# Kernel optimization log

Hardware: AMD Instinct MI355X
Metric: run time of the kernel (lower is better)

## Reference

```python
import jax, jax.numpy as jnp
import numpy as np
import math

B, S = 2, 2048
V, D, H, L, DFF = 1024, 512, 8, 6, 2048
DK = D // H
EPS = 1e-5


def _pos_encoding(seq_len, d_model, dtype):
    pos = jnp.arange(seq_len, dtype=jnp.float32)[:, None]
    div = jnp.exp(jnp.arange(0, d_model, 2, dtype=jnp.float32) * (-math.log(10000.0) / d_model))
    pe = jnp.zeros((seq_len, d_model), dtype=jnp.float32)
    pe = pe.at[:, 0::2].set(jnp.sin(pos * div))
    pe = pe.at[:, 1::2].set(jnp.cos(pos * div))
    return pe.astype(dtype)


def _layernorm(x, w, b):
    mu = jnp.mean(x, axis=-1, keepdims=True)
    var = jnp.mean(jnp.square(x - mu), axis=-1, keepdims=True)
    return (x - mu) * jax.lax.rsqrt(var + EPS) * w + b


def setup_inputs() -> dict:
    key = jax.random.key(0)
    ks = jax.random.split(key, 20)
    s = 0.02
    inp = {
        "input_ids": jax.random.randint(ks[0], (B, S), 1, V),
        "emb": jax.random.normal(ks[1], (V, D)) * s,
        # linear weights stored (in, out) so y = x @ W + b
        "wq": jax.random.normal(ks[2], (L, D, D)) * s,
        "bq": jnp.zeros((L, D)),
        "wk": jax.random.normal(ks[3], (L, D, D)) * s,
        "bk": jnp.zeros((L, D)),
        "wv": jax.random.normal(ks[4], (L, D, D)) * s,
        "bv": jnp.zeros((L, D)),
        "wo": jax.random.normal(ks[5], (L, D, D)) * (s / math.sqrt(2 * L)),
        "bo": jnp.zeros((L, D)),
        "ln1_w": jnp.ones((L, D)), "ln1_b": jnp.zeros((L, D)),
        "ln2_w": jnp.ones((L, D)), "ln2_b": jnp.zeros((L, D)),
        "w1": jax.random.normal(ks[6], (L, D, DFF)) * s,
        "b1": jnp.zeros((L, DFF)),
        "w2": jax.random.normal(ks[7], (L, DFF, D)) * (s / math.sqrt(2 * L)),
        "b2": jnp.zeros((L, D)),
        "out_w": jax.random.normal(ks[8], (D, V)) * s,
        "out_b": jnp.zeros((V,)),
    }
    return inp


def reference(input_ids, emb, wq, bq, wk, bk, wv, bv, wo, bo,
              ln1_w, ln1_b, ln2_w, ln2_b, w1, b1, w2, b2, out_w, out_b):
    pad_mask = (input_ids != 0)                              # [B,S] attend where True
    x = emb[input_ids]                                       # [B,S,D]
    x = x + _pos_encoding(S, D, x.dtype)[None, :, :]
    causal = jnp.tril(jnp.ones((S, S), dtype=bool))          # [S,S]
    mask = causal[None, None, :, :] & pad_mask[:, None, None, :]  # [B,1,S,S]
    scale = 1.0 / math.sqrt(DK)
    for l in range(L):
        h = _layernorm(x, ln1_w[l], ln1_b[l])
        q = (h @ wq[l] + bq[l]).reshape(B, S, H, DK)
        k = (h @ wk[l] + bk[l]).reshape(B, S, H, DK)
        v = (h @ wv[l] + bv[l]).reshape(B, S, H, DK)
        scores = jnp.einsum('bqhd,bkhd->bhqk', q, k) * scale
        scores = jnp.where(mask, scores, -jnp.inf)
        attn = jax.nn.softmax(scores, axis=-1)
        o = jnp.einsum('bhqk,bkhd->bqhd', attn, v).reshape(B, S, D)
        x = o @ wo[l] + bo[l]                                # NOTE: no residual on attention (faithful)
        h2 = _layernorm(x, ln2_w[l], ln2_b[l])
        ff = jax.nn.relu(h2 @ w1[l] + b1[l]) @ w2[l] + b2[l]
        x = x + ff
    logits = x @ out_w + out_b                               # [B,S,V]
    return logits
```

## Files before the change

kernel.cpp:

```cpp
#include <hip/hip_runtime.h>
#include <hip/hip_bf16.h>

#define B_ 2
#define S_ 2048
#define V_ 1024
#define D_ 512
#define H_ 8
#define L_ 6
#define DFF_ 2048
#define DK_ 64
#define MROWS (B_*S_)
#define NEGINF (-__builtin_inff())

typedef __hip_bfloat16 bf16;
typedef __bf16 bf16x8 __attribute__((ext_vector_type(8)));
typedef float f32x4 __attribute__((ext_vector_type(4)));
typedef unsigned short us8 __attribute__((ext_vector_type(8)));
typedef unsigned short us2 __attribute__((ext_vector_type(2)));

__device__ __forceinline__ float bf2f(unsigned short u) {
    return __uint_as_float(((unsigned int)u) << 16);
}
__device__ __forceinline__ unsigned short f2b(float x) {
    unsigned int u = __float_as_uint(x);
    return (unsigned short)((u + 0x7FFFu + ((u >> 16) & 1u)) >> 16);
}
__device__ __forceinline__ float ldin(const void* p, size_t i, int bf) {
    return bf ? bf2f(((const unsigned short*)p)[i]) : ((const float*)p)[i];
}

__global__ void detect_kernel(const unsigned int* __restrict__ w, int* __restrict__ flag) {
    if (threadIdx.x == 0) flag[0] = (w[0] == 0x3F800000u) ? 0 : 1;
}

__global__ __launch_bounds__(256) void embed_kernel(const int* __restrict__ ids,
        const void* __restrict__ emb, float* __restrict__ x, const int* __restrict__ dtf)
{
    const int bf = dtf[0];
    int tid = blockIdx.x * 256 + threadIdx.x;
    int d = tid % D_;
    int bs = tid / D_;
    int s = bs % S_;
    int id = ids[bs];
    float e = ldin(emb, (size_t)id * D_ + d, bf);
    int i2 = d & ~1;
    float div = expf((float)i2 * (-9.210340371976184f / (float)D_));
    float ang = (float)s * div;
    float pe = (d & 1) ? cosf(ang) : sinf(ang);
    x[tid] = e + pe;
}

__global__ __launch_bounds__(256) void ln_kernel(const float* __restrict__ x,
        const void* __restrict__ w, const void* __restrict__ b, size_t off,
        unsigned short* __restrict__ out, const int* __restrict__ dtf)
{
    const int bf = dtf[0];
    __shared__ float red[256];
    const int row = blockIdx.x;
    const int tid = threadIdx.x;
    const float* xr = x + (size_t)row * D_;
    float v0 = xr[tid], v1 = xr[tid + 256];
    red[tid] = v0 + v1; __syncthreads();
    for (int s = 128; s > 0; s >>= 1) { if (tid < s) red[tid] += red[tid + s]; __syncthreads(); }
    float mu = red[0] * (1.f / D_); __syncthreads();
    float d0 = v0 - mu, d1 = v1 - mu;
    red[tid] = d0 * d0 + d1 * d1; __syncthreads();
    for (int s = 128; s > 0; s >>= 1) { if (tid < s) red[tid] += red[tid + s]; __syncthreads(); }
    float var = red[0] * (1.f / D_);
    float rstd = rsqrtf(var + 1e-5f);
    unsigned short* orow = out + (size_t)row * D_;
    orow[tid]       = f2b(d0 * rstd * ldin(w, off + tid, bf)       + ldin(b, off + tid, bf));
    orow[tid + 256] = f2b(d1 * rstd * ldin(w, off + tid + 256, bf) + ldin(b, off + tid + 256, bf));
}

__device__ __forceinline__ void tr_tile(const void* src, size_t off, int K, int N,
        unsigned short* dst, int k0, int n0, int bf, unsigned short (*T)[72])
{
    const int t = threadIdx.x;
    const int r = t >> 2, c = (t & 3) * 16;
    size_t e = off + (size_t)(k0 + r) * N + n0 + c;
    us8 u0, u1;
    if (bf) {
        u0 = *(const us8*)((const unsigned short*)src + e);
        u1 = *(const us8*)((const unsigned short*)src + e + 8);
    } else {
        const float* p = (const float*)src + e;
        float4 f0 = *(const float4*)p, f1 = *(const float4*)(p + 4);
        float4 f2 = *(const float4*)(p + 8), f3 = *(const float4*)(p + 12);
        u0[0]=f2b(f0.x); u0[1]=f2b(f0.y); u0[2]=f2b(f0.z); u0[3]=f2b(f0.w);
        u0[4]=f2b(f1.x); u0[5]=f2b(f1.y); u0[6]=f2b(f1.z); u0[7]=f2b(f1.w);
        u1[0]=f2b(f2.x); u1[1]=f2b(f2.y); u1[2]=f2b(f2.z); u1[3]=f2b(f2.w);
        u1[4]=f2b(f3.x); u1[5]=f2b(f3.y); u1[6]=f2b(f3.z); u1[7]=f2b(f3.w);
    }
    *(us8*)&T[r][c] = u0;
    *(us8*)&T[r][c + 8] = u1;
    __syncthreads();
    us8 o0, o1;
    #pragma unroll
    for (int i = 0; i < 8; ++i) { o0[i] = T[c + i][r]; o1[i] = T[c + 8 + i][r]; }
    *(us8*)&dst[(size_t)(n0 + r) * K + k0 + c] = o0;
    *(us8*)&dst[(size_t)(n0 + r) * K + k0 + c + 8] = o1;
}

__global__ __launch_bounds__(256) void transpose_all(
        const void* wq, const void* wk, const void* wv, const void* wo,
        const void* w1, const void* w2,
        unsigned short* twq, unsigned short* twk, unsigned short* twv, unsigned short* two,
        unsigned short* tw1, unsigned short* tw2,
        int lbase, int slotmul, const int* __restrict__ dtf)
{
    __shared__ __align__(16) unsigned short T[64][72];
    const int bf = dtf[0];
    const int lrel = blockIdx.x / 768;
    const int within = blockIdx.x % 768;
    const int layer = lbase + lrel;
    const int slot = lrel * slotmul;
    const size_t offQ = (size_t)layer * D_ * D_;
    const size_t offF = (size_t)layer * D_ * DFF_;
    const size_t sQ = (size_t)slot * D_ * D_;
    const size_t sF = (size_t)slot * D_ * DFF_;
    if (within < 256) {
        int sel = within >> 6, tile = within & 63;
        const void* s = sel == 0 ? wq : sel == 1 ? wk : sel == 2 ? wv : wo;
        unsigned short* d = (sel == 0 ? twq : sel == 1 ? twk : sel == 2 ? twv : two) + sQ;
        tr_tile(s, offQ, D_, D_, d, (tile & 7) * 64, (tile >> 3) * 64, bf, T);
    } else if (within < 512) {
        int tile = within - 256;
        tr_tile(w1, offF, D_, DFF_, tw1 + sF, (tile & 7) * 64, (tile >> 3) * 64, bf, T);
    } else {
        int tile = within - 512;
        tr_tile(w2, offF, DFF_, D_, tw2 + sF, (tile & 31) * 64, (tile >> 5) * 64, bf, T);
    }
}

__global__ __launch_bounds__(256) void transpose_one(const void* src, size_t off,
        int K, int N, unsigned short* dst, const int* __restrict__ dtf)
{
    __shared__ __align__(16) unsigned short T[64][72];
    int tile = blockIdx.x;
    int tk = K / 64;
    tr_tile(src, off, K, N, dst, (tile % tk) * 64, (tile / tk) * 64, dtf[0], T);
}

template<bool ABF16, int OUTM, bool RELU, bool ADD>
__device__ __forceinline__ void gemm_core64(
        const void* __restrict__ A, const unsigned short* __restrict__ Wt,
        const void* __restrict__ bias, size_t bOff, const float* __restrict__ Res,
        void* __restrict__ Cout, int M, int N, int K, int bf)
{
    __shared__ __align__(16) unsigned short At[64][72];
    __shared__ __align__(16) unsigned short Bt[64][72];
    const int tid = threadIdx.x;
    const int wave = tid >> 6, lane = tid & 63;
    const int quad = lane >> 4, l16 = lane & 15;
    const int wm = (wave >> 1) * 32, wn = (wave & 1) * 32;
    const int n0 = blockIdx.x * 64, m0 = blockIdx.y * 64;
    const int r = tid >> 2, cb = tid & 3;

    f32x4 acc[2][2];
    #pragma unroll
    for (int mt = 0; mt < 2; ++mt)
        #pragma unroll
        for (int nt = 0; nt < 2; ++nt)
            acc[mt][nt] = (f32x4){0.f, 0.f, 0.f, 0.f};

    us8 aR[2], wR[2];
    float4 aF[4];

    auto loadT = [&](int k0) {
        if (ABF16) {
            const unsigned short* Ap = (const unsigned short*)A + (size_t)(m0 + r) * K + k0;
            aR[0] = *(const us8*)(Ap + cb * 8);
            aR[1] = *(const us8*)(Ap + (cb + 4) * 8);
        } else {
            const float* Ap = (const float*)A + (size_t)(m0 + r) * K + k0;
            aF[0] = *(const float4*)(Ap + cb * 8);
            aF[1] = *(const float4*)(Ap + cb * 8 + 4);
            aF[2] = *(const float4*)(Ap + (cb + 4) * 8);
            aF[3] = *(const float4*)(Ap + (cb + 4) * 8 + 4);
        }
        const unsigned short* Wp = Wt + (size_t)(n0 + r) * K + k0;
        wR[0] = *(const us8*)(Wp + cb * 8);
        wR[1] = *(const us8*)(Wp + (cb + 4) * 8);
    };
    auto storeT = [&]() {
        if (ABF16) {
            *(us8*)&At[r][cb * 8] = aR[0];
            *(us8*)&At[r][(cb + 4) * 8] = aR[1];
        } else {
            us8 u0, u1;
            u0[0]=f2b(aF[0].x); u0[1]=f2b(aF[0].y); u0[2]=f2b(aF[0].z); u0[3]=f2b(aF[0].w);
            u0[4]=f2b(aF[1].x); u0[5]=f2b(aF[1].y); u0[6]=f2b(aF[1].z); u0[7]=f2b(aF[1].w);
            u1[0]=f2b(aF[2].x); u1[1]=f2b(aF[2].y); u1[2]=f2b(aF[2].z); u1[3]=f2b(aF[2].w);
            u1[4]=f2b(aF[3].x); u1[5]=f2b(aF[3].y); u1[6]=f2b(aF[3].z); u1[7]=f2b(aF[3].w);
            *(us8*)&At[r][cb * 8] = u0;
            *(us8*)&At[r][(cb + 4) * 8] = u1;
        }
        *(us8*)&Bt[r][cb * 8] = wR[0];
        *(us8*)&Bt[r][(cb + 4) * 8] = wR[1];
    };

    loadT(0);
    for (int k0 = 0; k0 < K; k0 += 64) {
        __syncthreads();
        storeT();
        __syncthreads();
        if (k0 + 64 < K) loadT(k0 + 64);
        bf16x8 af[2][2], bw[2][2];
        #pragma unroll
        for (int mt = 0; mt < 2; ++mt)
            #pragma unroll
            for (int kh = 0; kh < 2; ++kh)
                af[mt][kh] = *(const bf16x8*)&At[wm + mt * 16 + l16][kh * 32 + quad * 8];
        #pragma unroll
        for (int nt = 0; nt < 2; ++nt)
            #pragma unroll
            for (int kh = 0; kh < 2; ++kh)
                bw[nt][kh] = *(const bf16x8*)&Bt[wn + nt * 16 + l16][kh * 32 + quad * 8];
        #pragma unroll
        for (int mt = 0; mt < 2; ++mt)
            #pragma unroll
            for (int nt = 0; nt < 2; ++nt) {
                acc[mt][nt] = __builtin_amdgcn_mfma_f32_16x16x32_bf16(af[mt][0], bw[nt][0], acc[mt][nt], 0, 0, 0);
                acc[mt][nt] = __builtin_amdgcn_mfma_f32_16x16x32_bf16(af[mt][1], bw[nt][1], acc[mt][nt], 0, 0, 0);
            }
    }

    #pragma unroll
    for (int mt = 0; mt < 2; ++mt) {
        #pragma unroll
        for (int nt = 0; nt < 2; ++nt) {
            int col = n0 + wn + nt * 16 + l16;
            float bv = ldin(bias, bOff + col, bf);
            #pragma unroll
            for (int rr = 0; rr < 4; ++rr) {
                int row = m0 + wm + mt * 16 + quad * 4 + rr;
                float c = acc[mt][nt][rr] + bv;
                if (ADD) c += Res[(size_t)row * N + col];
                if (RELU) c = fmaxf(c, 0.f);
                if (OUTM == 0)      ((float*)Cout)[(size_t)row * N + col] = c;
                else if (OUTM == 1) ((unsigned short*)Cout)[(size_t)row * N + col] = f2b(c);
                else {
                    if (bf) ((unsigned short*)Cout)[(size_t)row * N + col] = f2b(c);
                    else    ((float*)Cout)[(size_t)row * N + col] = c;
                }
            }
        }
    }
}

template<bool ABF16, int OUTM, bool RELU, bool ADD>
__global__ __launch_bounds__(256) void gemm64(
        const void* __restrict__ A, const unsigned short* __restrict__ Wt,
        const void* __restrict__ bias, size_t bOff, const float* __restrict__ Res,
        void* __restrict__ Cout, int M, int N, int K, const int* __restrict__ dtf)
{
    gemm_core64<ABF16, OUTM, RELU, ADD>(A, Wt, bias, bOff, Res, Cout, M, N, K, dtf[0]);
}

__global__ __launch_bounds__(256) void gemm_qkv64(
        const unsigned short* __restrict__ h,
        const unsigned short* twq, const unsigned short* twk, const unsigned short* twv,
        const void* bq, const void* bk, const void* bv, size_t bOff,
        unsigned short* q, unsigned short* k, unsigned short* v,
        const int* __restrict__ dtf)
{
    const int z = blockIdx.z;
    const unsigned short* W = (z == 0) ? twq : (z == 1) ? twk : twv;
    const void* bias = (z == 0) ? bq : (z == 1) ? bk : bv;
    unsigned short* out = (z == 0) ? q : (z == 1) ? k : v;
    gemm_core64<true, 1, false, false>(h, W, bias, bOff, nullptr, out, MROWS, D_, D_, dtf[0]);
}

__global__ __launch_bounds__(512) void attn_flash_v5(
        const unsigned short* __restrict__ qb, const unsigned short* __restrict__ kb,
        const unsigned short* __restrict__ vb, const int* __restrict__ ids,
        unsigned short* __restrict__ ob)
{
    __shared__ __align__(16) unsigned short Qs[2][64][72];
    __shared__ __align__(16) unsigned short Ks[4][64][72];
    __shared__ __align__(16) unsigned short Vt[4][64][72];
    __shared__ __align__(16) unsigned short Ps[2][64][72];
    __shared__ float Msk[S_];
    const int tid = threadIdx.x;
    const int grp = tid >> 8;
    const int t = tid & 255;
    const int wave = t >> 6, lane = t & 63;
    const int quad = lane >> 4, l16 = lane & 15;
    const int p = blockIdx.x, h = blockIdx.y, bz = blockIdx.z;
    const int a = p, bqt = 31 - p;
    const int qt_mine = grp ? bqt : a;
    const size_t hb = (size_t)bz * S_ * D_ + (size_t)h * DK_;
    const int sr = t >> 2, scq = (t & 3) * 16;
    const int pr = t >> 3, cvb = t & 7;

    const int kcols = (bqt + 1) * 64;
    for (int i = tid; i < kcols; i += 512)
        Msk[i] = (ids[bz * S_ + i] == 0) ? NEGINF : 0.f;

    {
        const unsigned short* qp = qb + hb + (size_t)(qt_mine * 64 + sr) * D_ + scq;
        *(us8*)&Qs[grp][sr][scq]     = *(const us8*)qp;
        *(us8*)&Qs[grp][sr][scq + 8] = *(const us8*)(qp + 8);
    }

    us8 kR0, kR1, vA, vB;
    auto loadKV1 = [&](int kt) {
        if (grp == 0) {
            const unsigned short* kp = kb + hb + (size_t)(kt * 64 + sr) * D_ + scq;
            kR0 = *(const us8*)kp;
            kR1 = *(const us8*)(kp + 8);
        } else {
            const unsigned short* vp = vb + hb + (size_t)(kt * 64 + 2 * pr) * D_ + cvb * 8;
            vA = *(const us8*)vp;
            vB = *(const us8*)(vp + D_);
        }
    };
    auto storeKV1 = [&](int buf) {
        if (grp == 0) {
            *(us8*)&Ks[buf][sr][scq]     = kR0;
            *(us8*)&Ks[buf][sr][scq + 8] = kR1;
        } else {
            #pragma unroll
            for (int i = 0; i < 8; ++i) {
                int ii = (i + cvb) & 7;
                us2 u2 = { vA[ii], vB[ii] };
                *(us2*)&Vt[buf][cvb * 8 + ii][2 * pr] = u2;
            }
        }
    };
    auto loadKV2 = [&](int kt) {
        const unsigned short* kp = kb + hb + (size_t)(kt * 64 + sr) * D_ + scq;
        kR0 = *(const us8*)kp;
        kR1 = *(const us8*)(kp + 8);
        const unsigned short* vp = vb + hb + (size_t)(kt * 64 + 2 * pr) * D_ + cvb * 8;
        vA = *(const us8*)vp;
        vB = *(const us8*)(vp + D_);
    };
    auto storeKV2 = [&](int buf) {
        *(us8*)&Ks[buf][sr][scq]     = kR0;
        *(us8*)&Ks[buf][sr][scq + 8] = kR1;
        #pragma unroll
        for (int i = 0; i < 8; ++i) {
            int ii = (i + cvb) & 7;
            us2 u2 = { vA[ii], vB[ii] };
            *(us2*)&Vt[buf][cvb * 8 + ii][2 * pr] = u2;
        }
    };

    f32x4 Oa[4];
    float m[4], l[4];
    #pragma unroll
    for (int r = 0; r < 4; ++r) { m[r] = NEGINF; l[r] = 0.f; }
    #pragma unroll
    for (int dt = 0; dt < 4; ++dt) Oa[dt] = (f32x4){0.f, 0.f, 0.f, 0.f};

    auto stepCompute = [&](int qsel, int kt, int buf, bool causal) {
        f32x4 sa[4];
        #pragma unroll
        for (int nt = 0; nt < 4; ++nt) sa[nt] = (f32x4){0.f, 0.f, 0.f, 0.f};
        #pragma unroll
        for (int ks = 0; ks < 2; ++ks) {
            bf16x8 aq = *(const bf16x8*)&Qs[qsel][wave * 16 + l16][ks * 32 + quad * 8];
            #pragma unroll
            for (int nt = 0; nt < 4; ++nt) {
                bf16x8 bk = *(const bf16x8*)&Ks[buf][nt * 16 + l16][ks * 32 + quad * 8];
                sa[nt] = __builtin_amdgcn_mfma_f32_16x16x32_bf16(aq, bk, sa[nt], 0, 0, 0);
            }
        }
        #pragma unroll
        for (int r = 0; r < 4; ++r) {
            float sv[4];
            #pragma unroll
            for (int nt = 0; nt < 4; ++nt) {
                float s = sa[nt][r] * 0.125f + Msk[kt * 64 + nt * 16 + l16];
                if (causal && (nt * 16 + l16) > (wave * 16 + quad * 4 + r)) s = NEGINF;
                sv[nt] = s;
            }
            float rmax = fmaxf(fmaxf(sv[0], sv[1]), fmaxf(sv[2], sv[3]));
            #pragma unroll
            for (int off = 8; off > 0; off >>= 1)
                rmax = fmaxf(rmax, __shfl_xor(rmax, off, 16));
            float mnew = fmaxf(m[r], rmax);
            float alpha = __expf(m[r] - mnew);
            float pv[4];
            float rsum = 0.f;
            #pragma unroll
            for (int nt = 0; nt < 4; ++nt) { pv[nt] = __expf(sv[nt] - mnew); rsum += pv[nt]; }
            #pragma unroll
            for (int off = 8; off > 0; off >>= 1)
                rsum += __shfl_xor(rsum, off, 16);
            l[r] = l[r] * alpha + rsum;
            m[r] = mnew;
            #pragma unroll
            for (int dt = 0; dt < 4; ++dt) Oa[dt][r] *= alpha;
            int prow = wave * 16 + quad * 4 + r;
            #pragma unroll
            for (int nt = 0; nt < 4; ++nt)
                Ps[grp][prow][nt * 16 + l16] = f2b(pv[nt]);
        }
        #pragma unroll
        for (int ks = 0; ks < 2; ++ks) {
            bf16x8 ap = *(const bf16x8*)&Ps[grp][wave * 16 + l16][ks * 32 + quad * 8];
            #pragma unroll
            for (int dt = 0; dt < 4; ++dt) {
                bf16x8 bv = *(const bf16x8*)&Vt[buf][dt * 16 + l16][ks * 32 + quad * 8];
                Oa[dt] = __builtin_amdgcn_mfma_f32_16x16x32_bf16(ap, bv, Oa[dt], 0, 0, 0);
            }
        }
    };
    auto writeOut = [&](int qt) {
        #pragma unroll
        for (int r = 0; r < 4; ++r) {
            float inv = 1.f / l[r];
            int row = qt * 64 + wave * 16 + quad * 4 + r;
            #pragma unroll
            for (int dt = 0; dt < 4; ++dt)
                ob[hb + (size_t)row * D_ + dt * 16 + l16] = f2b(Oa[dt][r] * inv);
        }
    };

    loadKV1(0);
    storeKV1(0);
    if (a >= 1) loadKV1(1);
    __syncthreads();

    #pragma unroll 1
    for (int kt = 0; kt <= a; ++kt) {
        const int cur = kt & 1;
        stepCompute(grp, kt, cur, kt == qt_mine);
        if (kt + 1 <= a) {
            storeKV1(cur ^ 1);
            if (kt + 2 <= a) loadKV1(kt + 2);
            __syncthreads();
        }
    }
    __syncthreads();

    if (grp == 0) {
        writeOut(a);
        #pragma unroll
        for (int r = 0; r < 4; ++r) { m[r] = NEGINF; l[r] = 0.f; }
        #pragma unroll
        for (int dt = 0; dt < 4; ++dt) Oa[dt] = (f32x4){0.f, 0.f, 0.f, 0.f};
    }

    const int nA = 15 - p, nSteps = 16 - p;
    auto activeP2 = [&](int step) { return grp ? (step < nSteps) : (step < nA); };
    auto ktP2 = [&](int step) { return grp ? (16 + step) : (p + 1 + step); };

    if (activeP2(0)) { loadKV2(ktP2(0)); storeKV2(2 * grp); }
    if (activeP2(1)) loadKV2(ktP2(1));
    __syncthreads();

    #pragma unroll 1
    for (int step = 0; step < nSteps; ++step) {
        if (activeP2(step))
            stepCompute(1, ktP2(step), 2 * grp + (step & 1), ktP2(step) == bqt);
        if (step + 1 < nSteps) {
            if (activeP2(step + 1)) storeKV2(2 * grp + ((step + 1) & 1));
            if (step + 2 < nSteps && activeP2(step + 2)) loadKV2(ktP2(step + 2));
        }
        __syncthreads();
    }

    float* Ob_ = (float*)&Qs[0][0][0];
    float* Ml_ = (float*)&Ps[0][0][0];
    if (grp == 0) {
        #pragma unroll
        for (int r = 0; r < 4; ++r) { Ml_[t * 4 + r] = m[r]; Ml_[1024 + t * 4 + r] = l[r]; }
        #pragma unroll
        for (int dt = 0; dt < 4; ++dt) *(f32x4*)&Ob_[(dt * 256 + t) * 4] = Oa[dt];
    }
    __syncthreads();
    if (grp == 1) {
        #pragma unroll
        for (int r = 0; r < 4; ++r) {
            float mA = Ml_[t * 4 + r], lA = Ml_[1024 + t * 4 + r];
            float mN = fmaxf(m[r], mA);
            float eB = __expf(m[r] - mN), eA = __expf(mA - mN);
            l[r] = l[r] * eB + lA * eA;
            m[r] = mN;
            #pragma unroll
            for (int dt = 0; dt < 4; ++dt)
                Oa[dt][r] = Oa[dt][r] * eB + Ob_[(dt * 256 + t) * 4 + r] * eA;
        }
        writeOut(bqt);
    }
}

extern "C" void kernel_launch(void* const* d_in, const int* in_sizes, int n_in,
                              void* d_out, int out_size, void* d_ws, size_t ws_size,
                              hipStream_t stream)
{
    const int* ids  = (const int*)d_in[0];
    const void* emb = d_in[1];
    const void* wq  = d_in[2];
    const void* bq  = d_in[3];
    const void* wk  = d_in[4];
    const void* bk  = d_in[5];
    const void* wv  = d_in[6];
    const void* bv  = d_in[7];
    const void* wo  = d_in[8];
    const void* bo  = d_in[9];
    const void* ln1w = d_in[10];
    const void* ln1b = d_in[11];
    const void* ln2w = d_in[12];
    const void* ln2b = d_in[13];
    const void* w1  = d_in[14];
    const void* b1  = d_in[15];
    const void* w2  = d_in[16];
    const void* b2  = d_in[17];
    const void* outw = d_in[18];
    const void* outb = d_in[19];

    char* wsp = (char*)d_ws;
    int* dtf = (int*)wsp;
    const size_t NROW = (size_t)MROWS * D_;

    const size_t fixedBytes = 256
        + 2 * NROW * 4
        + 5 * NROW * 2
        + (size_t)MROWS * DFF_ * 2
        + (size_t)D_ * V_ * 2;
    const size_t perLayerW = (4 * (size_t)D_ * D_ + 2 * (size_t)D_ * DFF_) * 2;
    const int slots = (ws_size >= fixedBytes + 6 * perLayerW) ? 6 : 1;

    float* xA = (float*)(wsp + 256);
    float* xB = xA + NROW;
    unsigned short* h  = (unsigned short*)(xB + NROW);
    unsigned short* q  = h + NROW;
    unsigned short* k  = q + NROW;
    unsigned short* v  = k + NROW;
    unsigned short* o  = v + NROW;
    unsigned short* ff = o + NROW;
    unsigned short* twout = ff + (size_t)MROWS * DFF_;
    unsigned short* twq = twout + (size_t)D_ * V_;
    unsigned short* twk = twq + (size_t)slots * D_ * D_;
    unsigned short* twv = twk + (size_t)slots * D_ * D_;
    unsigned short* two = twv + (size_t)slots * D_ * D_;
    unsigned short* tw1 = two + (size_t)slots * D_ * D_;
    unsigned short* tw2 = tw1 + (size_t)slots * D_ * DFF_;

    detect_kernel<<<1, 64, 0, stream>>>((const unsigned int*)ln1w, dtf);
    transpose_one<<<(D_/64) * (V_/64), 256, 0, stream>>>(outw, 0, D_, V_, twout, dtf);
    if (slots == 6)
        transpose_all<<<6 * 768, 256, 0, stream>>>(wq, wk, wv, wo, w1, w2,
            twq, twk, twv, two, tw1, tw2, 0, 1, dtf);
    embed_kernel<<<(MROWS * D_) / 256, 256, 0, stream>>>(ids, emb, xA, dtf);

    for (int l = 0; l < L_; ++l) {
        const size_t bOff = (size_t)l * D_;
        const int s = (slots == 6) ? l : 0;
        if (slots == 1)
            transpose_all<<<768, 256, 0, stream>>>(wq, wk, wv, wo, w1, w2,
                twq, twk, twv, two, tw1, tw2, l, 0, dtf);
        const unsigned short* lwq = twq + (size_t)s * D_ * D_;
        const unsigned short* lwk = twk + (size_t)s * D_ * D_;
        const unsigned short* lwv = twv + (size_t)s * D_ * D_;
        const unsigned short* lwo = two + (size_t)s * D_ * D_;
        const unsigned short* lw1 = tw1 + (size_t)s * D_ * DFF_;
        const unsigned short* lw2 = tw2 + (size_t)s * D_ * DFF_;

        ln_kernel<<<MROWS, 256, 0, stream>>>(xA, ln1w, ln1b, bOff, h, dtf);
        gemm_qkv64<<<dim3(D_/64, MROWS/64, 3), 256, 0, stream>>>(
            h, lwq, lwk, lwv, bq, bk, bv, bOff, q, k, v, dtf);
        attn_flash_v5<<<dim3(S_/128, H_, B_), 512, 0, stream>>>(q, k, v, ids, o);
        gemm64<true, 0, false, false><<<dim3(D_/64, MROWS/64), 256, 0, stream>>>(
            o, lwo, bo, bOff, nullptr, xB, MROWS, D_, D_, dtf);
        ln_kernel<<<MROWS, 256, 0, stream>>>(xB, ln2w, ln2b, bOff, h, dtf);
        gemm64<true, 1, true, false><<<dim3(DFF_/64, MROWS/64), 256, 0, stream>>>(
            h, lw1, b1, (size_t)l * DFF_, nullptr, ff, MROWS, DFF_, D_, dtf);
        gemm64<true, 0, false, true><<<dim3(D_/64, MROWS/64), 256, 0, stream>>>(
            ff, lw2, b2, bOff, xB, xA, MROWS, D_, DFF_, dtf);
    }
    gemm64<false, 2, false, false><<<dim3(V_/64, MROWS/64), 256, 0, stream>>>(
        xA, twout, outb, 0, nullptr, d_out, MROWS, V_, D_, dtf);
}
```

Before: 1.037 ms.

## Use 128x64 GEMM tiles with direct global-to-LDS async loads for layer GEMMs

Adds a new GEMM core with a 128x64 block tile. Each wave computes a 64x32 sub-tile, and global_load_lds moves A and weight tiles straight into shared memory without a register round-trip. The next k-slice is issued after the fragments are read into registers, so the load overlaps the MFMAs. The QKV, output-projection and both FFN GEMMs now use this core; the final logits GEMM keeps the 64 tile. The LDS layout is unpadded with a 64-element stride, which risks bank conflicts on the fragment reads, and the grid halves, which may reduce occupancy for the N=512 GEMMs.

```diff
diff --git a/kernel.cpp b/kernel.cpp
--- a/kernel.cpp
+++ b/kernel.cpp
@@ -27,6 +27,12 @@
 }
 __device__ __forceinline__ float ldin(const void* p, size_t i, int bf) {
     return bf ? bf2f(((const unsigned short*)p)[i]) : ((const float*)p)[i];
+}
+
+__device__ __forceinline__ void gload16(const void* g, void* l) {
+    __builtin_amdgcn_global_load_lds(
+        (const __attribute__((address_space(1))) unsigned int*)g,
+        (__attribute__((address_space(3))) unsigned int*)l, 16, 0, 0);
 }
 
 __global__ void detect_kernel(const unsigned int* __restrict__ w, int* __restrict__ flag) {
@@ -142,6 +148,106 @@
     tr_tile(src, off, K, N, dst, (tile % tk) * 64, (tile / tk) * 64, dtf[0], T);
 }
 
+template<int OUTM, bool RELU, bool ADD>
+__device__ __forceinline__ void gemm_core128(
+        const unsigned short* __restrict__ A, const unsigned short* __restrict__ Wt,
+        const void* __restrict__ bias, size_t bOff, const float* __restrict__ Res,
+        void* __restrict__ Cout, int M, int N, int K, int bf)
+{
+    __shared__ __align__(16) unsigned short As[128 * 64];
+    __shared__ __align__(16) unsigned short Bs[64 * 64];
+    const int tid = threadIdx.x;
+    const int wave = tid >> 6, lane = tid & 63;
+    const int quad = lane >> 4, l16 = lane & 15;
+    const int wm = (wave >> 1) * 64, wn = (wave & 1) * 32;
+    const int n0 = blockIdx.x * 64, m0 = blockIdx.y * 128;
+    const int arow = tid >> 3, acol = (tid & 7) * 8;
+
+    f32x4 acc[4][2];
+    #pragma unroll
+    for (int mt = 0; mt < 4; ++mt)
+        #pragma unroll
+        for (int nt = 0; nt < 2; ++nt)
+            acc[mt][nt] = (f32x4){0.f, 0.f, 0.f, 0.f};
+
+    auto stage = [&](int k0) {
+        #pragma unroll
+        for (int j = 0; j < 4; ++j)
+            gload16(A + (size_t)(m0 + j * 32 + arow) * K + k0 + acol,
+                    As + j * 2048 + wave * 512);
+        #pragma unroll
+        for (int j = 0; j < 2; ++j)
+            gload16(Wt + (size_t)(n0 + j * 32 + arow) * K + k0 + acol,
+                    Bs + j * 2048 + wave * 512);
+    };
+
+    stage(0);
+    for (int k0 = 0; k0 < K; k0 += 64) {
+        __syncthreads();
+        bf16x8 af[4][2], bw[2][2];
+        #pragma unroll
+        for (int mt = 0; mt < 4; ++mt)
+            #pragma unroll
+            for (int ks = 0; ks < 2; ++ks)
+                af[mt][ks] = *(const bf16x8*)&As[(wm + mt * 16 + l16) * 64 + ks * 32 + quad * 8];
+        #pragma unroll
+        for (int nt = 0; nt < 2; ++nt)
+            #pragma unroll
+            for (int ks = 0; ks < 2; ++ks)
+                bw[nt][ks] = *(const bf16x8*)&Bs[(wn + nt * 16 + l16) * 64 + ks * 32 + quad * 8];
+        __syncthreads();
+        if (k0 + 64 < K) stage(k0 + 64);
+        #pragma unroll
+        for (int mt = 0; mt < 4; ++mt)
+            #pragma unroll
+            for (int nt = 0; nt < 2; ++nt) {
+                acc[mt][nt] = __builtin_amdgcn_mfma_f32_16x16x32_bf16(af[mt][0], bw[nt][0], acc[mt][nt], 0, 0, 0);
+                acc[mt][nt] = __builtin_amdgcn_mfma_f32_16x16x32_bf16(af[mt][1], bw[nt][1], acc[mt][nt], 0, 0, 0);
+            }
+    }
+
+    #pragma unroll
+    for (int nt = 0; nt < 2; ++nt) {
+        int col = n0 + wn + nt * 16 + l16;
+        float bv = ldin(bias, bOff + col, bf);
+        #pragma unroll
+        for (int mt = 0; mt < 4; ++mt) {
+            #pragma unroll
+            for (int rr = 0; rr < 4; ++rr) {
+                int row = m0 + wm + mt * 16 + quad * 4 + rr;
+                float c = acc[mt][nt][rr] + bv;
+                if (ADD) c += Res[(size_t)row * N + col];
+                if (RELU) c = fmaxf(c, 0.f);
+                if (OUTM == 0) ((float*)Cout)[(size_t)row * N + col] = c;
+                else           ((unsigned short*)Cout)[(size_t)row * N + col] = f2b(c);
+            }
+        }
+    }
+}
+
+template<int OUTM, bool RELU, bool ADD>
+__global__ __launch_bounds__(256) void gemm128(
+        const unsigned short* __restrict__ A, const unsigned short* __restrict__ Wt,
+        const void* __restrict__ bias, size_t bOff, const float* __restrict__ Res,
+        void* __restrict__ Cout, int M, int N, int K, const int* __restrict__ dtf)
+{
+    gemm_core128<OUTM, RELU, ADD>(A, Wt, bias, bOff, Res, Cout, M, N, K, dtf[0]);
+}
+
+__global__ __launch_bounds__(256) void gemm_qkv128(
+        const unsigned short* __restrict__ h,
+        const unsigned short* twq, const unsigned short* twk, const unsigned short* twv,
+        const void* bq, const void* bk, const void* bv, size_t bOff,
+        unsigned short* q, unsigned short* k, unsigned short* v,
+        const int* __restrict__ dtf)
+{
+    const int z = blockIdx.z;
+    const unsigned short* W = (z == 0) ? twq : (z == 1) ? twk : twv;
+    const void* bias = (z == 0) ? bq : (z == 1) ? bk : bv;
+    unsigned short* out = (z == 0) ? q : (z == 1) ? k : v;
+    gemm_core128<1, false, false>(h, W, bias, bOff, nullptr, out, MROWS, D_, D_, dtf[0]);
+}
+
 template<bool ABF16, int OUTM, bool RELU, bool ADD>
 __device__ __forceinline__ void gemm_core64(
         const void* __restrict__ A, const unsigned short* __restrict__ Wt,
@@ -256,20 +362,6 @@
         void* __restrict__ Cout, int M, int N, int K, const int* __restrict__ dtf)
 {
     gemm_core64<ABF16, OUTM, RELU, ADD>(A, Wt, bias, bOff, Res, Cout, M, N, K, dtf[0]);
-}
-
-__global__ __launch_bounds__(256) void gemm_qkv64(
-        const unsigned short* __restrict__ h,
-        const unsigned short* twq, const unsigned short* twk, const unsigned short* twv,
-        const void* bq, const void* bk, const void* bv, size_t bOff,
-        unsigned short* q, unsigned short* k, unsigned short* v,
-        const int* __restrict__ dtf)
-{
-    const int z = blockIdx.z;
-    const unsigned short* W = (z == 0) ? twq : (z == 1) ? twk : twv;
-    const void* bias = (z == 0) ? bq : (z == 1) ? bk : bv;
-    unsigned short* out = (z == 0) ? q : (z == 1) ? k : v;
-    gemm_core64<true, 1, false, false>(h, W, bias, bOff, nullptr, out, MROWS, D_, D_, dtf[0]);
 }
 
 __global__ __launch_bounds__(512) void attn_flash_v5(
@@ -563,15 +655,15 @@
         const unsigned short* lw2 = tw2 + (size_t)s * D_ * DFF_;
 
         ln_kernel<<<MROWS, 256, 0, stream>>>(xA, ln1w, ln1b, bOff, h, dtf);
-        gemm_qkv64<<<dim3(D_/64, MROWS/64, 3), 256, 0, stream>>>(
+        gemm_qkv128<<<dim3(D_/64, MROWS/128, 3), 256, 0, stream>>>(
             h, lwq, lwk, lwv, bq, bk, bv, bOff, q, k, v, dtf);
         attn_flash_v5<<<dim3(S_/128, H_, B_), 512, 0, stream>>>(q, k, v, ids, o);
-        gemm64<true, 0, false, false><<<dim3(D_/64, MROWS/64), 256, 0, stream>>>(
+        gemm128<0, false, false><<<dim3(D_/64, MROWS/128), 256, 0, stream>>>(
             o, lwo, bo, bOff, nullptr, xB, MROWS, D_, D_, dtf);
         ln_kernel<<<MROWS, 256, 0, stream>>>(xB, ln2w, ln2b, bOff, h, dtf);
-        gemm64<true, 1, true, false><<<dim3(DFF_/64, MROWS/64), 256, 0, stream>>>(
+        gemm128<1, true, false><<<dim3(DFF_/64, MROWS/128), 256, 0, stream>>>(
             h, lw1, b1, (size_t)l * DFF_, nullptr, ff, MROWS, DFF_, D_, dtf);
-        gemm64<true, 0, false, true><<<dim3(D_/64, MROWS/64), 256, 0, stream>>>(
+        gemm128<0, false, true><<<dim3(D_/64, MROWS/128), 256, 0, stream>>>(
             ff, lw2, b2, bOff, xB, xA, MROWS, D_, DFF_, dtf);
     }
     gemm64<false, 2, false, false><<<dim3(V_/64, MROWS/64), 256, 0, stream>>>(
```

Measured after the change: 1.129 ms. 1.09x slower.
